# Kernel optimization log

Hardware: AMD Instinct MI355X
Metric: run time of the kernel (lower is better)

## Reference

```python
import jax, jax.numpy as jnp
import numpy as np

NT, NF, CIN, COUT = 1_500_000, 500_000, 32, 32
BN_EPS = 1e-5


def setup_inputs() -> dict:
    key = jax.random.key(0)
    k1, k2, k3 = jax.random.split(key, 3)
    input_texture = jax.random.normal(k1, (NT, CIN), dtype=jnp.float32)
    # barycentric coefficients: nonnegative, rows sum to 1
    b = jax.random.uniform(k2, (NT, 3), dtype=jnp.float32) + 1e-3
    bary_coeff = b / b.sum(axis=1, keepdims=True)
    # 3 texture samples per facet (sum == NT)
    num_texture = jnp.full((NF,), 3, dtype=jnp.int32)
    # xavier-normal init for [Cout, Cin, 3] kernel
    fan = CIN * 3 + COUT * 3
    std = float(np.sqrt(2.0 / fan))
    weights = jax.random.normal(k3, (COUT, CIN, 3), dtype=jnp.float32) * std
    bias = jnp.zeros((1, COUT), dtype=jnp.float32)
    gamma = jnp.ones((COUT,), dtype=jnp.float32)
    beta = jnp.zeros((COUT,), dtype=jnp.float32)
    return {"input_texture": input_texture, "bary_coeff": bary_coeff,
            "num_texture": num_texture, "weights": weights, "bias": bias,
            "gamma": gamma, "beta": beta}


def reference(input_texture, bary_coeff, num_texture, weights, bias, gamma, beta):
    nf = num_texture.shape[0]
    nt = input_texture.shape[0]
    # segment id for each ragged texture sample (original op uses cumsum offsets)
    seg = jnp.repeat(jnp.arange(nf), num_texture, total_repeat_length=nt)
    # per-sample contribution: y[t,o] = sum_{c,k} x[t,c] * b[t,k] * W[o,c,k]
    y = jnp.einsum('tc,tk,ock->to', input_texture, bary_coeff, weights)
    # facet2facet averages over the samples of each facet
    s = jax.ops.segment_sum(y, seg, num_segments=nf)  # [Nf, Cout]
    cnt = jnp.maximum(num_texture.astype(y.dtype), 1)[:, None]
    out = s / cnt
    out = out + bias          # bias add
    out = jax.nn.relu(out)    # activation
    # BatchNorm1d in training mode: batch statistics over the facet dim
    mean = out.mean(axis=0)
    var = out.var(axis=0)
    out = (out - mean) * jax.lax.rsqrt(var + BN_EPS) * gamma + beta
    return out
```

## Files before the change

kernel.cpp:

```cpp
#include <hip/hip_runtime.h>
#include <hip/hip_bf16.h>
#include <stdint.h>

typedef __attribute__((ext_vector_type(4))) float fv4;
typedef float fv4u __attribute__((ext_vector_type(4), aligned(4)));
typedef __attribute__((ext_vector_type(4))) short sv4;
typedef __attribute__((ext_vector_type(8))) short sv8;

#define SCHUNK 2048
#define NIT 8
#define SPAN (64 * NIT)
#define PZB 108

static __device__ __forceinline__ short f2bf(float f) {
  __hip_bfloat16 h = __float2bfloat16(f);
  union { __hip_bfloat16 h; short s; } u; u.h = h;
  return u.s;
}

__global__ __launch_bounds__(256) void scan1(const int* __restrict__ num, int nf,
                                             int* __restrict__ bsum) {
  __shared__ int sd[256];
  int b = blockIdx.x, tid = threadIdx.x;
  int base = b * SCHUNK + tid * 8;
  int s = 0;
#pragma unroll
  for (int j = 0; j < 8; ++j) { int i = base + j; if (i < nf) s += num[i]; }
  sd[tid] = s; __syncthreads();
  for (int st = 128; st > 0; st >>= 1) {
    if (tid < st) sd[tid] += sd[tid + st];
    __syncthreads();
  }
  if (tid == 0) bsum[b] = sd[0];
}

__global__ __launch_bounds__(256) void scan2(int* __restrict__ bsum, int nb) {
  __shared__ int sd[256];
  int tid = threadIdx.x;
  int v = (tid < nb) ? bsum[tid] : 0;
  sd[tid] = v; __syncthreads();
  for (int off = 1; off < 256; off <<= 1) {
    int t = (tid >= off) ? sd[tid - off] : 0;
    __syncthreads();
    sd[tid] += t;
    __syncthreads();
  }
  if (tid < nb) bsum[tid] = sd[tid] - v;
}

__global__ __launch_bounds__(256) void scan3(const int* __restrict__ num, int nf,
                                             const int* __restrict__ bsum,
                                             int* __restrict__ offsets) {
  __shared__ int sc_[256];
  int b = blockIdx.x, tid = threadIdx.x;
  int base = b * SCHUNK + tid * 8;
  int loc[8]; int s = 0;
#pragma unroll
  for (int j = 0; j < 8; ++j) {
    loc[j] = (base + j < nf) ? num[base + j] : 0;
    s += loc[j];
  }
  sc_[tid] = s; __syncthreads();
  for (int off = 1; off < 256; off <<= 1) {
    int t = (tid >= off) ? sc_[tid - off] : 0;
    __syncthreads();
    sc_[tid] += t;
    __syncthreads();
  }
  int run = bsum[b] + sc_[tid] - s;
#pragma unroll
  for (int j = 0; j < 8; ++j) {
    if (base + j < nf) offsets[base + j] = run;
    run += loc[j];
  }
  if (b == gridDim.x - 1 && tid == 255) offsets[nf] = run;
}

__global__ __launch_bounds__(256, 4) void k_main(
    const float* __restrict__ x, const float* __restrict__ bary,
    const float* __restrict__ W, const float* __restrict__ bias,
    const int* __restrict__ offsets, float* __restrict__ out,
    float* __restrict__ partials, int nf, int nt, int nw)
{
  __shared__ short W2[32 * PZB];

  const int tid = threadIdx.x;
  const int lane = tid & 63;
  const int wv = tid >> 6;

  for (int idx = tid; idx < 3072; idx += 256) {
    int o = idx / 96;
    int ck = idx - o * 96;
    int k = ck >> 5, c = ck & 31;
    W2[o * PZB + ck] = f2bf(W[o * 96 + c * 3 + k]);
  }
  __syncthreads();

  const int rowl = lane & 15;
  const int grp = lane >> 4;
  const int cb_lo = grp * 4;
  const int cb_hi = grp * 4 + 16;
  const int blk0 = blockIdx.x * SPAN;

  sv8 bfrA[3], bfrB[3];
#pragma unroll
  for (int kb = 0; kb < 3; ++kb) {
    const int cko = kb * 32 + grp * 4;
    {
      const short* wr = &W2[rowl * PZB + cko];
      sv4 lo = *(const sv4*)(wr), hi = *(const sv4*)(wr + 16);
#pragma unroll
      for (int j = 0; j < 4; ++j) { bfrA[kb][j] = lo[j]; bfrA[kb][4 + j] = hi[j]; }
    }
    {
      const short* wr = &W2[(16 + rowl) * PZB + cko];
      sv4 lo = *(const sv4*)(wr), hi = *(const sv4*)(wr + 16);
#pragma unroll
      for (int j = 0; j < 4; ++j) { bfrB[kb][j] = lo[j]; bfrB[kb][4 + j] = hi[j]; }
    }
  }

  float bo0 = bias[rowl];
  float bo1 = bias[16 + rowl];
  float s1l = 0.f, s1h = 0.f, s2l = 0.f, s2h = 0.f;

#pragma unroll 2
  for (int t = 0; t < NIT; ++t) {
    const int f0t = blk0 + t * 64 + wv * 16;
    const int f = f0t + rowl;
    const int fa = f < nf ? f : nf;
    const int fb = (f + 1) < nf ? (f + 1) : nf;

    const int st = offsets[fa];
    const int en = offsets[fb];
    const int s3 = 3 * f;
    const int sbase = (f < nf && s3 + 3 <= nt) ? s3 : 0;
    const float* xp0 = x + (size_t)(sbase + 0) * 32;
    const float* xp1 = x + (size_t)(sbase + 1) * 32;
    const float* xp2 = x + (size_t)(sbase + 2) * 32;
    fv4 x0a = *(const fv4*)(xp0 + cb_lo), x0b = *(const fv4*)(xp0 + cb_hi);
    fv4 x1a = *(const fv4*)(xp1 + cb_lo), x1b = *(const fv4*)(xp1 + cb_hi);
    fv4 x2a = *(const fv4*)(xp2 + cb_lo), x2b = *(const fv4*)(xp2 + cb_hi);
    const float* bp = bary + (size_t)sbase * 3;
    fv4u bv0 = *(const fv4u*)(bp);
    fv4u bv1 = *(const fv4u*)(bp + 4);
    float b22 = bp[8];
    float b00 = bv0[0], b01 = bv0[1], b02 = bv0[2];
    float b10 = bv0[3], b11 = bv1[0], b12 = bv1[1];
    float b20 = bv1[2], b21 = bv1[3];

    const int nm_my = en - st;

    float z0[8], z1[8], z2[8];
#pragma unroll
    for (int j = 0; j < 8; ++j) { z0[j] = 0.f; z1[j] = 0.f; z2[j] = 0.f; }

    if (nm_my == 3 && st == s3) {
#pragma unroll
      for (int j = 0; j < 4; ++j) {
        z0[j]     += x0a[j] * b00; z1[j]     += x0a[j] * b01; z2[j]     += x0a[j] * b02;
        z0[4 + j] += x0b[j] * b00; z1[4 + j] += x0b[j] * b01; z2[4 + j] += x0b[j] * b02;
      }
#pragma unroll
      for (int j = 0; j < 4; ++j) {
        z0[j]     += x1a[j] * b10; z1[j]     += x1a[j] * b11; z2[j]     += x1a[j] * b12;
        z0[4 + j] += x1b[j] * b10; z1[4 + j] += x1b[j] * b11; z2[4 + j] += x1b[j] * b12;
      }
#pragma unroll
      for (int j = 0; j < 4; ++j) {
        z0[j]     += x2a[j] * b20; z1[j]     += x2a[j] * b21; z2[j]     += x2a[j] * b22;
        z0[4 + j] += x2b[j] * b20; z1[4 + j] += x2b[j] * b21; z2[4 + j] += x2b[j] * b22;
      }
    } else {
      for (int t2 = st; t2 < en; ++t2) {
        const float* xp = x + (size_t)t2 * 32;
        fv4 xa = *(const fv4*)(xp + cb_lo);
        fv4 xb = *(const fv4*)(xp + cb_hi);
        const float* bpp = bary + (size_t)t2 * 3;
        float b0 = bpp[0], b1 = bpp[1], b2 = bpp[2];
#pragma unroll
        for (int j = 0; j < 4; ++j) {
          z0[j]     += xa[j] * b0; z1[j]     += xa[j] * b1; z2[j]     += xa[j] * b2;
          z0[4 + j] += xb[j] * b0; z1[4 + j] += xb[j] * b1; z2[4 + j] += xb[j] * b2;
        }
      }
    }

    fv4 acc0 = (fv4){0.f, 0.f, 0.f, 0.f};
    fv4 acc1 = (fv4){0.f, 0.f, 0.f, 0.f};
#pragma unroll
    for (int kb = 0; kb < 3; ++kb) {
      sv8 afr;
#pragma unroll
      for (int j = 0; j < 4; ++j) {
        float lo = (kb == 0) ? z0[j]     : (kb == 1) ? z1[j]     : z2[j];
        float hi = (kb == 0) ? z0[4 + j] : (kb == 1) ? z1[4 + j] : z2[4 + j];
        afr[j]     = f2bf(lo);
        afr[4 + j] = f2bf(hi);
      }
      acc0 = __builtin_amdgcn_mfma_f32_16x16x32_bf16(afr, bfrA[kb], acc0, 0, 0, 0);
      acc1 = __builtin_amdgcn_mfma_f32_16x16x32_bf16(afr, bfrB[kb], acc1, 0, 0, 0);
    }

#pragma unroll
    for (int r = 0; r < 4; ++r) {
      int row = grp * 4 + r;
      int fr = f0t + row;
      int nm = __shfl(nm_my, row, 64);
      float inv = 1.0f / (float)(nm > 1 ? nm : 1);
      if (fr < nf) {
        float v0 = fmaxf(acc0[r] * inv + bo0, 0.f);
        float v1 = fmaxf(acc1[r] * inv + bo1, 0.f);
        out[fr * 32 + rowl]      = v0;
        out[fr * 32 + 16 + rowl] = v1;
        s1l += v0; s2l += v0 * v0;
        s1h += v1; s2h += v1 * v1;
      }
    }
  }

  s1l += __shfl_xor(s1l, 16, 64); s1l += __shfl_xor(s1l, 32, 64);
  s1h += __shfl_xor(s1h, 16, 64); s1h += __shfl_xor(s1h, 32, 64);
  s2l += __shfl_xor(s2l, 16, 64); s2l += __shfl_xor(s2l, 32, 64);
  s2h += __shfl_xor(s2h, 16, 64); s2h += __shfl_xor(s2h, 32, 64);
  if (grp == 0) {
    int w = blockIdx.x * 4 + wv;
    partials[(long)(rowl)      * nw + w] = s1l;
    partials[(long)(16 + rowl) * nw + w] = s1h;
    partials[(long)(32 + rowl) * nw + w] = s2l;
    partials[(long)(48 + rowl) * nw + w] = s2h;
  }
}

__global__ __launch_bounds__(256) void k_reduce(const float* __restrict__ partials,
                                                int nw, float* __restrict__ stats) {
  __shared__ float sd[256];
  int c = blockIdx.x;
  const float* p = partials + (long)c * nw;
  float s = 0.f;
  for (int i = threadIdx.x; i < nw; i += 256) s += p[i];
  sd[threadIdx.x] = s; __syncthreads();
  for (int st = 128; st > 0; st >>= 1) {
    if (threadIdx.x < st) sd[threadIdx.x] += sd[threadIdx.x + st];
    __syncthreads();
  }
  if (threadIdx.x == 0) stats[c] = sd[0];
}

__global__ __launch_bounds__(256) void k_bn(float* __restrict__ out,
                                            const float* __restrict__ stats,
                                            const float* __restrict__ gamma,
                                            const float* __restrict__ beta, int nf) {
  __shared__ float sc[32], sh[32];
  if (threadIdx.x < 32) {
    int o = threadIdx.x;
    float inv_n = 1.0f / (float)nf;
    float mean = stats[o] * inv_n;
    float var = stats[32 + o] * inv_n - mean * mean;
    float rstd = rsqrtf(var + 1e-5f);
    float g = gamma[o] * rstd;
    sc[o] = g;
    sh[o] = beta[o] - mean * g;
  }
  __syncthreads();
  long total4 = (long)nf * 8;
  long idx0 = (long)blockIdx.x * 256 + threadIdx.x;
  int ob = ((int)idx0 & 7) * 4;
  fv4 scv = *(const fv4*)&sc[ob];
  fv4 shv = *(const fv4*)&sh[ob];
  for (long idx = idx0; idx < total4; idx += (long)gridDim.x * 256) {
    fv4 v = *((const fv4*)out + idx);
    v = v * scv + shv;
    *((fv4*)out + idx) = v;
  }
}

extern "C" void kernel_launch(void* const* d_in, const int* in_sizes, int n_in,
                              void* d_out, int out_size, void* d_ws, size_t ws_size,
                              hipStream_t stream) {
  const float* x     = (const float*)d_in[0];
  const float* bary  = (const float*)d_in[1];
  const int*   numt  = (const int*)d_in[2];
  const float* W     = (const float*)d_in[3];
  const float* bias  = (const float*)d_in[4];
  const float* gamma = (const float*)d_in[5];
  const float* beta  = (const float*)d_in[6];
  float* out = (float*)d_out;

  const int nf   = in_sizes[2];
  const int nt   = in_sizes[0] / 32;
  const int nblk = (nf + SPAN - 1) / SPAN;
  const int nw   = nblk * 4;
  const int nbS  = (nf + SCHUNK - 1) / SCHUNK;

  char* w = (char*)d_ws;
  int* offsets = (int*)w;
  size_t off1 = (4UL * (size_t)(nf + 1) + 255) & ~255UL;
  int* bsum = (int*)(w + off1);
  size_t off2 = (off1 + 4UL * (size_t)nbS + 255) & ~255UL;
  float* partials = (float*)(w + off2);
  size_t off3 = (off2 + 4UL * 64UL * (size_t)nw + 255) & ~255UL;
  float* stats = (float*)(w + off3);

  scan1<<<nbS, 256, 0, stream>>>(numt, nf, bsum);
  scan2<<<1, 256, 0, stream>>>(bsum, nbS);
  scan3<<<nbS, 256, 0, stream>>>(numt, nf, bsum, offsets);
  k_main<<<nblk, 256, 0, stream>>>(x, bary, W, bias, offsets, out, partials, nf, nt, nw);
  k_reduce<<<64, 256, 0, stream>>>(partials, nw, stats);
  k_bn<<<2048, 256, 0, stream>>>(out, stats, gamma, beta, nf);
}
```

Baseline: 95.30 us.

## Precompute bf16 weights in a prep kernel and use single-wave blocks

Weight conversion to bf16 moves out of every block's shared-memory prologue into a one-block prep kernel that writes a global buffer, which k_main then reads directly. k_main becomes a 64-thread single-wave block handling 32 facets with no __syncthreads, which gives a much larger grid. The aim is to drop the per-block weight transpose and barrier and to improve load balance and latency hiding. In exchange it adds a kernel launch, multiplies the number of partial-stat entries so k_reduce has more work, and makes every wave reload the weights from global memory or cache.

```diff
diff --git a/kernel.cpp b/kernel.cpp
--- a/kernel.cpp
+++ b/kernel.cpp
@@ -8,9 +8,8 @@
 typedef __attribute__((ext_vector_type(8))) short sv8;
 
 #define SCHUNK 2048
-#define NIT 8
-#define SPAN (64 * NIT)
-#define PZB 108
+#define NIT 2
+#define SPAN (16 * NIT)
 
 static __device__ __forceinline__ short f2bf(float f) {
   __hip_bfloat16 h = __float2bfloat16(f);
@@ -76,26 +75,23 @@
   if (b == gridDim.x - 1 && tid == 255) offsets[nf] = run;
 }
 
-__global__ __launch_bounds__(256, 4) void k_main(
+__global__ __launch_bounds__(256) void k_prep(const float* __restrict__ W,
+                                              short* __restrict__ w2g) {
+  for (int i = threadIdx.x; i < 3072; i += 256) {
+    int o = i / 96;
+    int ck = i - o * 96;
+    int k = ck >> 5, c = ck & 31;
+    w2g[o * 96 + ck] = f2bf(W[o * 96 + c * 3 + k]);
+  }
+}
+
+__global__ __launch_bounds__(64, 4) void k_main(
     const float* __restrict__ x, const float* __restrict__ bary,
-    const float* __restrict__ W, const float* __restrict__ bias,
+    const short* __restrict__ w2g, const float* __restrict__ bias,
     const int* __restrict__ offsets, float* __restrict__ out,
     float* __restrict__ partials, int nf, int nt, int nw)
 {
-  __shared__ short W2[32 * PZB];
-
-  const int tid = threadIdx.x;
-  const int lane = tid & 63;
-  const int wv = tid >> 6;
-
-  for (int idx = tid; idx < 3072; idx += 256) {
-    int o = idx / 96;
-    int ck = idx - o * 96;
-    int k = ck >> 5, c = ck & 31;
-    W2[o * PZB + ck] = f2bf(W[o * 96 + c * 3 + k]);
-  }
-  __syncthreads();
-
+  const int lane = threadIdx.x & 63;
   const int rowl = lane & 15;
   const int grp = lane >> 4;
   const int cb_lo = grp * 4;
@@ -107,13 +103,13 @@
   for (int kb = 0; kb < 3; ++kb) {
     const int cko = kb * 32 + grp * 4;
     {
-      const short* wr = &W2[rowl * PZB + cko];
+      const short* wr = w2g + rowl * 96 + cko;
       sv4 lo = *(const sv4*)(wr), hi = *(const sv4*)(wr + 16);
 #pragma unroll
       for (int j = 0; j < 4; ++j) { bfrA[kb][j] = lo[j]; bfrA[kb][4 + j] = hi[j]; }
     }
     {
-      const short* wr = &W2[(16 + rowl) * PZB + cko];
+      const short* wr = w2g + (16 + rowl) * 96 + cko;
       sv4 lo = *(const sv4*)(wr), hi = *(const sv4*)(wr + 16);
 #pragma unroll
       for (int j = 0; j < 4; ++j) { bfrB[kb][j] = lo[j]; bfrB[kb][4 + j] = hi[j]; }
@@ -124,9 +120,9 @@
   float bo1 = bias[16 + rowl];
   float s1l = 0.f, s1h = 0.f, s2l = 0.f, s2h = 0.f;
 
-#pragma unroll 2
+#pragma unroll
   for (int t = 0; t < NIT; ++t) {
-    const int f0t = blk0 + t * 64 + wv * 16;
+    const int f0t = blk0 + t * 16;
     const int f = f0t + rowl;
     const int fa = f < nf ? f : nf;
     const int fb = (f + 1) < nf ? (f + 1) : nf;
@@ -224,7 +220,7 @@
   s2l += __shfl_xor(s2l, 16, 64); s2l += __shfl_xor(s2l, 32, 64);
   s2h += __shfl_xor(s2h, 16, 64); s2h += __shfl_xor(s2h, 32, 64);
   if (grp == 0) {
-    int w = blockIdx.x * 4 + wv;
+    int w = blockIdx.x;
     partials[(long)(rowl)      * nw + w] = s1l;
     partials[(long)(16 + rowl) * nw + w] = s1h;
     partials[(long)(32 + rowl) * nw + w] = s2l;
@@ -290,7 +286,7 @@
   const int nf   = in_sizes[2];
   const int nt   = in_sizes[0] / 32;
   const int nblk = (nf + SPAN - 1) / SPAN;
-  const int nw   = nblk * 4;
+  const int nw   = nblk;
   const int nbS  = (nf + SCHUNK - 1) / SCHUNK;
 
   char* w = (char*)d_ws;
@@ -298,14 +294,17 @@
   size_t off1 = (4UL * (size_t)(nf + 1) + 255) & ~255UL;
   int* bsum = (int*)(w + off1);
   size_t off2 = (off1 + 4UL * (size_t)nbS + 255) & ~255UL;
-  float* partials = (float*)(w + off2);
-  size_t off3 = (off2 + 4UL * 64UL * (size_t)nw + 255) & ~255UL;
-  float* stats = (float*)(w + off3);
+  short* w2g = (short*)(w + off2);
+  size_t off3 = (off2 + 2UL * 3072UL + 255) & ~255UL;
+  float* partials = (float*)(w + off3);
+  size_t off4 = (off3 + 4UL * 64UL * (size_t)nw + 255) & ~255UL;
+  float* stats = (float*)(w + off4);
 
   scan1<<<nbS, 256, 0, stream>>>(numt, nf, bsum);
   scan2<<<1, 256, 0, stream>>>(bsum, nbS);
   scan3<<<nbS, 256, 0, stream>>>(numt, nf, bsum, offsets);
-  k_main<<<nblk, 256, 0, stream>>>(x, bary, W, bias, offsets, out, partials, nf, nt, nw);
+  k_prep<<<1, 256, 0, stream>>>(W, w2g);
+  k_main<<<nblk, 64, 0, stream>>>(x, bary, w2g, bias, offsets, out, partials, nf, nt, nw);
   k_reduce<<<64, 256, 0, stream>>>(partials, nw, stats);
   k_bn<<<2048, 256, 0, stream>>>(out, stats, gamma, beta, nf);
 }
```

After: 120.5 us. 26.4% more time.
